# Kernel tuning notes

Measured on AMD Instinct MI355X. Metric: run time of the kernel, lower is better.

## Reference

```python
import jax, jax.numpy as jnp
import numpy as np


def setup_inputs() -> dict:
    key = jax.random.key(0)
    kZ, kQ, kW, kU, kbk = jax.random.split(key, 5)
    B, E, D = 64, 16, 64
    N_ATOMS = 200000
    N_NP = 160000
    N_BK = 20000
    Q_DIM = 64
    Z = jax.random.normal(kZ, (B, E, D), dtype=jnp.float32)
    Q = jax.random.normal(kQ, (B, Q_DIM), dtype=jnp.float32)
    W = jax.random.normal(kW, (N_NP, D), dtype=jnp.float32)
    U = jax.random.normal(kU, (N_NP, Q_DIM), dtype=jnp.float32)
    np_indices = jnp.arange(N_NP, dtype=jnp.int64 if jax.config.jax_enable_x64 else jnp.int32)
    bk_indices = jax.random.randint(kbk, (N_BK,), 0, N_ATOMS, dtype=jnp.int32)
    return {"Z": Z, "Q": Q, "W": W, "U": U,
            "np_indices": np_indices, "bk_indices": bk_indices,
            "n_atoms": N_ATOMS}


def reference(Z, Q, W, U, np_indices, bk_indices, n_atoms):
    # Batched valuation for all neural-predicate atoms at once:
    # vm(Z, Q, atom_i) = sigmoid(sum_{e,d} Z[b,e,d] * W[i,d] + Q[b] . U[i])
    scores = jax.nn.sigmoid(jnp.einsum('bed,nd->bn', Z, W) + Q @ U.T)  # [B, n_np]
    B = Z.shape[0]
    V = jnp.zeros((B, n_atoms), dtype=jnp.float32)
    V = V.at[:, 0].set(1.0)                 # V[:, 0] = 1.0 (true atom)
    V = V.at[:, np_indices].set(scores)     # scatter valuation outputs
    V = V.at[:, bk_indices].add(1.0)        # background knowledge atoms += 1
    return V
```

## Files before the change

### kernel.cpp

```cpp
#include <hip/hip_runtime.h>


typedef _Float16 half8_t __attribute__((ext_vector_type(8)));
typedef float float4_t __attribute__((ext_vector_type(4)));

#define E_DIM 16
#define D_DIM 64
#define QD    64
#define NS    2

__global__ void prep_kernel(const float* __restrict__ Z, const float* __restrict__ Q,
                            const int* __restrict__ bk, int n_bk,
                            _Float16* __restrict__ Afrag, float* __restrict__ cnt) {
    int blk = blockIdx.x;
    int tid = threadIdx.x;
    if (blk < 32) {
        int t = blk * 256 + tid;
        int b = t >> 7, k = t & 127;
        float v;
        if (k < D_DIM) {
            const float* zp = Z + (size_t)b * E_DIM * D_DIM + k;
            v = 0.f;
            #pragma unroll
            for (int e = 0; e < E_DIM; ++e) v += zp[e * D_DIM];
        } else {
            v = Q[b * QD + (k - D_DIM)];
        }
        int mt = b >> 4, r = b & 15;
        int kq = k >> 5, j = k & 7, quad = (k >> 3) & 3;
        int lane = r + quad * 16;
        Afrag[(((mt * 4 + kq) * 64) + lane) * 8 + j] = (_Float16)v;
    } else if (cnt) {
        int i = (blk - 32) * 256 + tid;
        if (i < n_bk) atomicAdd(&cnt[bk[i]], 1.0f);
    }
}

__global__ __launch_bounds__(256, 4) void main_kernel(
        const float* __restrict__ W, const float* __restrict__ U,
        const _Float16* __restrict__ Afrag, const float* __restrict__ cnt,
        float* __restrict__ V, int n_np, int n_atoms, int tail_w) {
    int tid = threadIdx.x;
    int bid = blockIdx.x;
    long long base = (long long)bid * (64 * NS);
    int wv = tid >> 6, lane = tid & 63;
    int quad = lane >> 4, l15 = lane & 15;
    int rB = wv * 16 + l15;

    const float4_t* Wg = (const float4_t*)W;
    const float4_t* Ug = (const float4_t*)U;
    const volatile half8_t* Ap = (const volatile half8_t*)Afrag;

    float4_t wraw[4], uraw[4];
    {
        size_t o = ((size_t)(base + rB)) * 16 + quad * 2;
        wraw[0] = Wg[o];     wraw[1] = Wg[o + 1];
        wraw[2] = Wg[o + 8]; wraw[3] = Wg[o + 9];
        uraw[0] = Ug[o];     uraw[1] = Ug[o + 1];
        uraw[2] = Ug[o + 8]; uraw[3] = Ug[o + 9];
    }

    {
        long long tb = (long long)n_np + (long long)bid * tail_w;
        int c8 = tid & 7, rg = tid >> 3;
        long long col = tb + 4 * c8;
        if (4 * c8 < tail_w && col < n_atoms) {
            float4_t cn4 = {0.f, 0.f, 0.f, 0.f};
            if (cnt) cn4 = *(const float4_t*)(cnt + col);
            *(float4_t*)(V + (size_t)rg * n_atoms + col) = cn4;
            *(float4_t*)(V + (size_t)(rg + 32) * n_atoms + col) = cn4;
        }
    }

    #pragma unroll
    for (int s = 0; s < NS; ++s) {
        long long colbase = base + s * 64;

        float cn = 0.f;
        if (cnt) cn = cnt[colbase + rB];

        half8_t b0, b1, b2, b3;
        #pragma unroll
        for (int q = 0; q < 4; ++q) {
            b0[q]     = (_Float16)wraw[0][q];
            b0[q + 4] = (_Float16)wraw[1][q];
            b1[q]     = (_Float16)wraw[2][q];
            b1[q + 4] = (_Float16)wraw[3][q];
            b2[q]     = (_Float16)uraw[0][q];
            b2[q + 4] = (_Float16)uraw[1][q];
            b3[q]     = (_Float16)uraw[2][q];
            b3[q + 4] = (_Float16)uraw[3][q];
        }

        if (s + 1 < NS) {
            size_t o = ((size_t)(base + (s + 1) * 64 + rB)) * 16 + quad * 2;
            wraw[0] = Wg[o];     wraw[1] = Wg[o + 1];
            wraw[2] = Wg[o + 8]; wraw[3] = Wg[o + 9];
            uraw[0] = Ug[o];     uraw[1] = Ug[o + 1];
            uraw[2] = Ug[o + 8]; uraw[3] = Ug[o + 9];
        }

        #pragma unroll
        for (int mt = 0; mt < 4; ++mt) {
            half8_t a0 = Ap[(mt * 4 + 0) * 64 + lane];
            half8_t a1 = Ap[(mt * 4 + 1) * 64 + lane];
            half8_t a2 = Ap[(mt * 4 + 2) * 64 + lane];
            half8_t a3 = Ap[(mt * 4 + 3) * 64 + lane];
            float4_t acc = {0.f, 0.f, 0.f, 0.f};
            acc = __builtin_amdgcn_mfma_f32_16x16x32_f16(a0, b0, acc, 0, 0, 0);
            acc = __builtin_amdgcn_mfma_f32_16x16x32_f16(a1, b1, acc, 0, 0, 0);
            acc = __builtin_amdgcn_mfma_f32_16x16x32_f16(a2, b2, acc, 0, 0, 0);
            acc = __builtin_amdgcn_mfma_f32_16x16x32_f16(a3, b3, acc, 0, 0, 0);
            float* vp = V + (size_t)(mt * 16 + quad * 4) * n_atoms + colbase + rB;
            #pragma unroll
            for (int r = 0; r < 4; ++r) {
                float sv = 1.0f / (1.0f + __expf(-acc[r])) + cn;
                vp[(size_t)r * n_atoms] = sv;
            }
        }
    }
}

__global__ void bk_scatter(const int* __restrict__ bk, int n_bk,
                           float* __restrict__ V, int n_atoms) {
    int i = blockIdx.x * 256 + threadIdx.x;
    if (i < n_bk)
        atomicAdd(&V[(size_t)blockIdx.y * n_atoms + bk[i]], 1.0f);
}

extern "C" void kernel_launch(void* const* d_in, const int* in_sizes, int n_in,
                              void* d_out, int out_size, void* d_ws, size_t ws_size,
                              hipStream_t stream) {
    const float* Z = (const float*)d_in[0];
    const float* Q = (const float*)d_in[1];
    const float* W = (const float*)d_in[2];
    const float* U = (const float*)d_in[3];
    const int* bk = (const int*)d_in[5];
    float* V = (float*)d_out;

    int B       = in_sizes[0] / (E_DIM * D_DIM);
    int n_np    = in_sizes[2] / D_DIM;
    int n_bk    = in_sizes[5];
    int n_atoms = out_size / B;

    _Float16* Afrag = (_Float16*)d_ws;
    size_t need = 16384 + (size_t)n_atoms * sizeof(float);
    bool use_cnt = ws_size >= need;
    float* cnt = use_cnt ? (float*)((char*)d_ws + 16384) : nullptr;

    if (use_cnt) {
        hipMemsetAsync(cnt, 0, (size_t)n_atoms * sizeof(float), stream);
        int cnt_blocks = (n_bk + 255) / 256;
        prep_kernel<<<32 + cnt_blocks, 256, 0, stream>>>(Z, Q, bk, n_bk, Afrag, cnt);
    } else {
        prep_kernel<<<32, 256, 0, stream>>>(Z, Q, bk, n_bk, Afrag, nullptr);
    }

    int gb = n_np / (64 * NS);
    int tail_w = (n_atoms - n_np + gb - 1) / gb;
    main_kernel<<<gb, 256, 0, stream>>>(W, U, Afrag, cnt, V,
                                        n_np, n_atoms, tail_w);

    if (!use_cnt) {
        dim3 g((n_bk + 255) / 256, B);
        bk_scatter<<<g, 256, 0, stream>>>(bk, n_bk, V, n_atoms);
    }
}
```

Baseline: 148.0 us.

## Use persistent grid-stride blocks with LDS-staged A fragments and double-buffered panels

The main kernel now launches a fixed number of persistent blocks. Each block loops over 64-column panels with grid stride and double-buffers the W/U register loads across iterations. The A fragments are staged once per block into shared memory instead of being re-read through volatile global loads, and the tail fill becomes a grid-stride loop. This aims to cut block launch overhead and repeated A loads, at the cost of fewer blocks in flight and a lower occupancy hint.

```diff
diff --git a/kernel.cpp b/kernel.cpp
--- a/kernel.cpp
+++ b/kernel.cpp
@@ -7,7 +7,6 @@
 #define E_DIM 16
 #define D_DIM 64
 #define QD    64
-#define NS    2
 
 __global__ void prep_kernel(const float* __restrict__ Z, const float* __restrict__ Q,
                             const int* __restrict__ bk, int n_bk,
@@ -36,88 +35,107 @@
     }
 }
 
-__global__ __launch_bounds__(256, 4) void main_kernel(
+__global__ __launch_bounds__(256, 3) void main_kernel(
         const float* __restrict__ W, const float* __restrict__ U,
         const _Float16* __restrict__ Afrag, const float* __restrict__ cnt,
-        float* __restrict__ V, int n_np, int n_atoms, int tail_w) {
+        float* __restrict__ V, int n_np, int n_atoms,
+        int n_panels, int n_blocks) {
+    __shared__ __align__(16) half8_t Ash[1024];
     int tid = threadIdx.x;
     int bid = blockIdx.x;
-    long long base = (long long)bid * (64 * NS);
     int wv = tid >> 6, lane = tid & 63;
     int quad = lane >> 4, l15 = lane & 15;
     int rB = wv * 16 + l15;
 
     const float4_t* Wg = (const float4_t*)W;
     const float4_t* Ug = (const float4_t*)U;
-    const volatile half8_t* Ap = (const volatile half8_t*)Afrag;
 
-    float4_t wraw[4], uraw[4];
     {
-        size_t o = ((size_t)(base + rB)) * 16 + quad * 2;
-        wraw[0] = Wg[o];     wraw[1] = Wg[o + 1];
-        wraw[2] = Wg[o + 8]; wraw[3] = Wg[o + 9];
-        uraw[0] = Ug[o];     uraw[1] = Ug[o + 1];
-        uraw[2] = Ug[o + 8]; uraw[3] = Ug[o + 9];
+        const half8_t* Ap = (const half8_t*)Afrag;
+        #pragma unroll
+        for (int i = 0; i < 4; ++i)
+            Ash[tid + i * 256] = Ap[tid + i * 256];
     }
 
     {
-        long long tb = (long long)n_np + (long long)bid * tail_w;
-        int c8 = tid & 7, rg = tid >> 3;
-        long long col = tb + 4 * c8;
-        if (4 * c8 < tail_w && col < n_atoms) {
+        long long ntail4 = (long long)(n_atoms - n_np) >> 2;
+        long long total  = 64 * ntail4;
+        long long stride = (long long)n_blocks * 256;
+        for (long long cidx = (long long)bid * 256 + tid; cidx < total;
+             cidx += stride) {
+            long long row = cidx / ntail4;
+            long long col = n_np + (cidx - row * ntail4) * 4;
             float4_t cn4 = {0.f, 0.f, 0.f, 0.f};
             if (cnt) cn4 = *(const float4_t*)(cnt + col);
-            *(float4_t*)(V + (size_t)rg * n_atoms + col) = cn4;
-            *(float4_t*)(V + (size_t)(rg + 32) * n_atoms + col) = cn4;
+            *(float4_t*)(V + (size_t)row * n_atoms + col) = cn4;
         }
     }
 
-    #pragma unroll
-    for (int s = 0; s < NS; ++s) {
-        long long colbase = base + s * 64;
+    __syncthreads();
 
-        float cn = 0.f;
-        if (cnt) cn = cnt[colbase + rB];
+    auto load_panel = [&](int p, float4_t wr[4], float4_t ur[4], float& cn) {
+        size_t o = ((size_t)p * 64 + rB) * 16 + quad * 2;
+        wr[0] = Wg[o];     wr[1] = Wg[o + 1];
+        wr[2] = Wg[o + 8]; wr[3] = Wg[o + 9];
+        ur[0] = Ug[o];     ur[1] = Ug[o + 1];
+        ur[2] = Ug[o + 8]; ur[3] = Ug[o + 9];
+        cn = 0.f;
+        if (cnt) cn = cnt[(size_t)p * 64 + rB];
+    };
 
+    auto compute_store = [&](int p, const float4_t wr[4], const float4_t ur[4],
+                             float cn) {
         half8_t b0, b1, b2, b3;
         #pragma unroll
         for (int q = 0; q < 4; ++q) {
-            b0[q]     = (_Float16)wraw[0][q];
-            b0[q + 4] = (_Float16)wraw[1][q];
-            b1[q]     = (_Float16)wraw[2][q];
-            b1[q + 4] = (_Float16)wraw[3][q];
-            b2[q]     = (_Float16)uraw[0][q];
-            b2[q + 4] = (_Float16)uraw[1][q];
-            b3[q]     = (_Float16)uraw[2][q];
-            b3[q + 4] = (_Float16)uraw[3][q];
+            b0[q]     = (_Float16)wr[0][q];
+            b0[q + 4] = (_Float16)wr[1][q];
+            b1[q]     = (_Float16)wr[2][q];
+            b1[q + 4] = (_Float16)wr[3][q];
+            b2[q]     = (_Float16)ur[0][q];
+            b2[q + 4] = (_Float16)ur[1][q];
+            b3[q]     = (_Float16)ur[2][q];
+            b3[q + 4] = (_Float16)ur[3][q];
         }
-
-        if (s + 1 < NS) {
-            size_t o = ((size_t)(base + (s + 1) * 64 + rB)) * 16 + quad * 2;
-            wraw[0] = Wg[o];     wraw[1] = Wg[o + 1];
-            wraw[2] = Wg[o + 8]; wraw[3] = Wg[o + 9];
-            uraw[0] = Ug[o];     uraw[1] = Ug[o + 1];
-            uraw[2] = Ug[o + 8]; uraw[3] = Ug[o + 9];
-        }
-
         #pragma unroll
         for (int mt = 0; mt < 4; ++mt) {
-            half8_t a0 = Ap[(mt * 4 + 0) * 64 + lane];
-            half8_t a1 = Ap[(mt * 4 + 1) * 64 + lane];
-            half8_t a2 = Ap[(mt * 4 + 2) * 64 + lane];
-            half8_t a3 = Ap[(mt * 4 + 3) * 64 + lane];
+            half8_t a0 = Ash[(mt * 4 + 0) * 64 + lane];
+            half8_t a1 = Ash[(mt * 4 + 1) * 64 + lane];
+            half8_t a2 = Ash[(mt * 4 + 2) * 64 + lane];
+            half8_t a3 = Ash[(mt * 4 + 3) * 64 + lane];
             float4_t acc = {0.f, 0.f, 0.f, 0.f};
             acc = __builtin_amdgcn_mfma_f32_16x16x32_f16(a0, b0, acc, 0, 0, 0);
             acc = __builtin_amdgcn_mfma_f32_16x16x32_f16(a1, b1, acc, 0, 0, 0);
             acc = __builtin_amdgcn_mfma_f32_16x16x32_f16(a2, b2, acc, 0, 0, 0);
             acc = __builtin_amdgcn_mfma_f32_16x16x32_f16(a3, b3, acc, 0, 0, 0);
-            float* vp = V + (size_t)(mt * 16 + quad * 4) * n_atoms + colbase + rB;
+            float* vp = V + (size_t)(mt * 16 + quad * 4) * n_atoms
+                          + (size_t)p * 64 + rB;
             #pragma unroll
             for (int r = 0; r < 4; ++r) {
                 float sv = 1.0f / (1.0f + __expf(-acc[r])) + cn;
                 vp[(size_t)r * n_atoms] = sv;
             }
         }
+    };
+
+    int p = bid;
+    if (p >= n_panels) return;
+    float4_t wA[4], uA[4], wB[4], uB[4];
+    float cnA, cnB;
+    load_panel(p, wA, uA, cnA);
+    for (;;) {
+        int pn = p + n_blocks;
+        bool more = pn < n_panels;
+        if (more) load_panel(pn, wB, uB, cnB);
+        compute_store(p, wA, uA, cnA);
+        if (!more) break;
+        p = pn;
+        pn = p + n_blocks;
+        more = pn < n_panels;
+        if (more) load_panel(pn, wA, uA, cnA);
+        compute_store(p, wB, uB, cnB);
+        if (!more) break;
+        p = pn;
     }
 }
 
@@ -156,10 +174,11 @@
         prep_kernel<<<32, 256, 0, stream>>>(Z, Q, bk, n_bk, Afrag, nullptr);
     }
 
-    int gb = n_np / (64 * NS);
-    int tail_w = (n_atoms - n_np + gb - 1) / gb;
-    main_kernel<<<gb, 256, 0, stream>>>(W, U, Afrag, cnt, V,
-                                        n_np, n_atoms, tail_w);
+    int n_panels = n_np / 64;
+    int n_blocks = 625;
+    if (n_blocks > n_panels) n_blocks = n_panels;
+    main_kernel<<<n_blocks, 256, 0, stream>>>(W, U, Afrag, cnt, V,
+                                              n_np, n_atoms, n_panels, n_blocks);
 
     if (!use_cnt) {
         dim3 g((n_bk + 255) / 256, B);
```

After: 151.1 us. +2.1%, slower.
